# Performance work log

Hardware: AMD Instinct MI355X
Metric: run time of the kernel (lower is better)

## Reference

```python
import jax, jax.numpy as jnp
import numpy as np

L, V, D = 8, 512, 256            # num_loci, per-locus vocab, embedding_dim
B, K = 8192, 16                  # batch, candidates per sample
HID = 2 * D                      # pooling MLP hidden width


def setup_inputs() -> dict:
    key = jax.random.key(0)
    k_tok, k_tab, k_w1, k_w2 = jax.random.split(key, 4)
    haplotypes = jax.random.randint(k_tok, (B, K, L), 0, V, dtype=jnp.int64)
    # nn.Embedding default init: N(0, 1); padding_idx row zeroed.
    tables = jax.random.normal(k_tab, (L, V, D), dtype=jnp.float32)
    tables = tables.at[:, 0, :].set(0.0)
    # Xavier-uniform for the two Linear layers (stored as [in, out]).
    lim1 = float(np.sqrt(6.0 / (L * D + HID)))
    W1 = jax.random.uniform(k_w1, (L * D, HID), jnp.float32, -lim1, lim1)
    b1 = jnp.zeros((HID,), jnp.float32)
    lim2 = float(np.sqrt(6.0 / (HID + D)))
    W2 = jax.random.uniform(k_w2, (HID, D), jnp.float32, -lim2, lim2)
    b2 = jnp.zeros((D,), jnp.float32)
    return {"haplotypes": haplotypes, "tables": tables,
            "W1": W1, "b1": b1, "W2": W2, "b2": b2}


def reference(haplotypes, tables, W1, b1, W2, b2):
    b, k, num_loci = haplotypes.shape
    vocab = tables.shape[1]
    tok = jnp.clip(haplotypes.reshape(-1, num_loci), 0, vocab - 1)  # [N, L]
    # Per-locus gather, vectorized over loci: [N, L, D]
    emb = tables[jnp.arange(num_loci), tok]
    # padding_idx row is all-zeros; masking keeps forward identical and
    # matches torch's zero-gradient behavior for the padding row.
    emb = emb * (tok != 0)[..., None].astype(emb.dtype)
    x = emb.reshape(emb.shape[0], num_loci * tables.shape[2])  # concat -> [N, L*D]
    h = jax.nn.gelu(x @ W1 + b1, approximate=False)            # torch GELU = erf
    out = h @ W2 + b2                                          # [N, D]
    return out.reshape(b, k, tables.shape[2])
```

## Files before the change

kernel.cpp:

```cpp
#include <hip/hip_runtime.h>
#include <math.h>

typedef __attribute__((ext_vector_type(8))) short  short8;
typedef __attribute__((ext_vector_type(4))) float  floatx4;
typedef __attribute__((ext_vector_type(2))) float  float2v;
typedef __attribute__((ext_vector_type(4))) unsigned int uintx4;

#define NLOCI 8
#define VOCAB 512
#define DDIM  256
#define HID   512
#define NSAMP (8192 * 16)

__device__ __forceinline__ float bitsf(unsigned int u) {
    union { unsigned int u; float f; } c; c.u = u; return c.f;
}
__device__ __forceinline__ unsigned short f2bf(float f) {
    union { float f; unsigned int u; } c; c.f = f;
    unsigned int u = c.u;
    return (unsigned short)((u + 0x7FFFu + ((u >> 16) & 1u)) >> 16);
}
__device__ __forceinline__ unsigned short f2bf_fast(float f) {
    union { float f; unsigned int u; } c; c.f = f;
    return (unsigned short)((c.u + 0x8000u) >> 16);
}
__device__ __forceinline__ float gelu_fast(float x) {
    float t = x * x;
    float y = x * __builtin_fmaf(0.035677408f, t, 0.79788456f);
    float e = __builtin_amdgcn_exp2f(y * 2.8853901f);
    float r = __builtin_amdgcn_rcpf(e + 1.0f);
    return x - x * r;
}
__device__ __forceinline__ void async_copy16(const void* g, void* l) {
    __builtin_amdgcn_global_load_lds(
        (const __attribute__((address_space(1))) unsigned int*)g,
        (__attribute__((address_space(3))) unsigned int*)l, 16, 0, 0);
}

__device__ __forceinline__ short8 sum_gelu(const uintx4* g) {
    short8 afrag;
#pragma unroll
    for (int j = 0; j < 4; ++j) {
        float2v u0 = (float2v){bitsf(g[0][j] << 16), bitsf(g[0][j] & 0xFFFF0000u)};
        float2v u1 = (float2v){bitsf(g[1][j] << 16), bitsf(g[1][j] & 0xFFFF0000u)};
        float2v u2 = (float2v){bitsf(g[2][j] << 16), bitsf(g[2][j] & 0xFFFF0000u)};
        float2v u3 = (float2v){bitsf(g[3][j] << 16), bitsf(g[3][j] & 0xFFFF0000u)};
        float2v u4 = (float2v){bitsf(g[4][j] << 16), bitsf(g[4][j] & 0xFFFF0000u)};
        float2v u5 = (float2v){bitsf(g[5][j] << 16), bitsf(g[5][j] & 0xFFFF0000u)};
        float2v u6 = (float2v){bitsf(g[6][j] << 16), bitsf(g[6][j] & 0xFFFF0000u)};
        float2v u7 = (float2v){bitsf(g[7][j] << 16), bitsf(g[7][j] & 0xFFFF0000u)};
        float2v sj = ((u0 + u1) + (u2 + u3)) + ((u4 + u5) + (u6 + u7));
        afrag[2 * j]     = (short)f2bf_fast(gelu_fast(sj[0]));
        afrag[2 * j + 1] = (short)f2bf_fast(gelu_fast(sj[1]));
    }
    return afrag;
}

__global__ __launch_bounds__(256) void k_prep(
    const float* __restrict__ tables,
    const float* __restrict__ W1,
    const float* __restrict__ b1,
    const float* __restrict__ W2,
    unsigned short* __restrict__ Tp,
    unsigned short* __restrict__ W2t)
{
    __shared__ unsigned short a_lds[64 * 256];
    __shared__ unsigned short bt_lds[64 * 256];

    const int t = threadIdx.x;

    if (blockIdx.x >= 512) {
        const int bid = blockIdx.x - 512;
        const int r0 = (bid & 7) * 64;
        const int c0 = (bid >> 3) * 64;
        float* tile = (float*)a_lds;
#pragma unroll
        for (int i = 0; i < 16; ++i) {
            int flat = i * 256 + t;
            int rr = flat >> 6, cc = flat & 63;
            tile[rr * 65 + cc] = W2[(r0 + rr) * DDIM + c0 + cc];
        }
        __syncthreads();
#pragma unroll
        for (int i = 0; i < 8; ++i) {
            int flat = i * 256 + t;
            int cc = flat >> 5, rp = (flat & 31) * 2;
            ushort2 v;
            v.x = f2bf(tile[rp * 65 + cc]);
            v.y = f2bf(tile[(rp + 1) * 65 + cc]);
            *(ushort2*)(W2t + (c0 + cc) * HID + r0 + rp) = v;
        }
        return;
    }

    const int l  = blockIdx.x >> 6;
    const int v0 = ((blockIdx.x >> 3) & 7) * 64;
    const int n0 = (blockIdx.x & 7) * 64;

    {
        const float* asrc = tables + (l * 512 + v0) * 256;
#pragma unroll
        for (int i = 0; i < 16; ++i) {
            int flat = i * 1024 + t * 4;
            int row = flat >> 8, k = flat & 255;
            float4 v = *(const float4*)(asrc + flat);
            ushort4 pk4;
            pk4.x = f2bf(v.x); pk4.y = f2bf(v.y); pk4.z = f2bf(v.z); pk4.w = f2bf(v.w);
            int chunkX = (k >> 3) ^ (row & 31);
            *(ushort4*)(a_lds + row * 256 + chunkX * 8 + (k & 7)) = pk4;
        }
    }
    {
        const int n = t & 63;
        const int kq = (t >> 6) * 64;
        const float* bsrc = W1 + (l * 256) * 512 + n0 + n;
#pragma unroll
        for (int i = 0; i < 8; ++i) {
            int k0 = kq + i * 8;
            short8 pk8;
#pragma unroll
            for (int j = 0; j < 8; ++j)
                pk8[j] = (short)f2bf(bsrc[(k0 + j) * 512]);
            int chunkX = (k0 >> 3) ^ (n & 31);
            *(short8*)(bt_lds + n * 256 + chunkX * 8) = pk8;
        }
    }
    __syncthreads();

    const int wave = t >> 6, lane = t & 63;
    const int p = lane & 15, q = lane >> 4;
    const int arow = wave * 16 + p;

    floatx4 acc[4];
#pragma unroll
    for (int nt = 0; nt < 4; ++nt) acc[nt] = (floatx4){0.f, 0.f, 0.f, 0.f};

#pragma unroll
    for (int kc = 0; kc < 8; ++kc) {
        int cq = kc * 4 + q;
        short8 afrag = *(const short8*)(a_lds + arow * 256 + (cq ^ (arow & 31)) * 8);
#pragma unroll
        for (int nt = 0; nt < 4; ++nt) {
            int brow = nt * 16 + p;
            short8 bfrag = *(const short8*)(bt_lds + brow * 256 + (cq ^ (brow & 31)) * 8);
            acc[nt] = __builtin_amdgcn_mfma_f32_16x16x32_bf16(afrag, bfrag, acc[nt], 0, 0, 0);
        }
    }

#pragma unroll
    for (int nt = 0; nt < 4; ++nt) {
        int col = n0 + nt * 16 + p;
        float badd = (l == 0) ? b1[col] : 0.0f;
#pragma unroll
        for (int r = 0; r < 4; ++r) {
            int row = v0 + wave * 16 + q * 4 + r;
            Tp[(l * 512 + row) * 512 + col] = f2bf(acc[nt][r] + badd);
        }
    }
}

__global__ __launch_bounds__(256, 3) void k_main(
    const int* __restrict__ hap,
    const unsigned short* __restrict__ Tp,
    const unsigned short* __restrict__ W2t,
    const float* __restrict__ b2,
    float* __restrict__ out)
{
    __shared__ unsigned short w2_lds[256 * 64];

    const int t = threadIdx.x;
    const int wave = t >> 6, lane = t & 63;
    const int p = lane & 15, q = lane >> 4;
    const int m_base = blockIdx.x * 64 + wave * 16;

    unsigned int goff[8];
    {
        const uintx4* hp = (const uintx4*)(hap + (m_base + p) * 8);
        uintx4 h0 = hp[0], h1 = hp[1];
#pragma unroll
        for (int l = 0; l < 4; ++l) {
            goff[l]     = (unsigned)(l)     * 524288u + (h0[l] & 511u) * 1024u + (unsigned)(q * 32);
            goff[l + 4] = (unsigned)(l + 4) * 524288u + (h1[l] & 511u) * 1024u + (unsigned)(q * 32);
        }
    }
    const char* Tpc = (const char*)Tp;

    const int drow = lane >> 3;
    const int j_sw = (lane & 7) ^ (drow & 7);
    const unsigned short* wsrc = W2t + (wave * 64 + drow) * 512 + j_sw * 8;
    const int p7 = p & 7;

    floatx4 acc[16];
#pragma unroll
    for (int nt = 0; nt < 16; ++nt) acc[nt] = (floatx4){0.f, 0.f, 0.f, 0.f};

    uintx4 ga0[8], ga1[8];
#pragma unroll
    for (int l = 0; l < 8; ++l)
        ga0[l] = *(const uintx4*)(Tpc + goff[l]);
#pragma unroll
    for (int l = 0; l < 8; ++l)
        ga1[l] = *(const uintx4*)(Tpc + goff[l] + 16);
    __builtin_amdgcn_sched_barrier(0);

#pragma unroll
    for (int kb = 0; kb < 8; ++kb) {
        asm volatile("s_waitcnt lgkmcnt(0)" ::: "memory");
        __builtin_amdgcn_s_barrier();
        __builtin_amdgcn_sched_barrier(0);
#pragma unroll
        for (int i = 0; i < 8; ++i)
            async_copy16(wsrc + kb * 64 + i * 8 * 512,
                         w2_lds + (wave * 64 + i * 8) * 64);
        __builtin_amdgcn_sched_barrier(0);

        asm volatile("s_waitcnt vmcnt(16)" ::: "memory");
        short8 afrag0 = sum_gelu(ga0);
        __builtin_amdgcn_sched_barrier(0);

        if (kb < 7) {
#pragma unroll
            for (int l = 0; l < 8; ++l)
                ga0[l] = *(const uintx4*)(Tpc + goff[l] + (kb + 1) * 128);
            __builtin_amdgcn_sched_barrier(0);
        }

        if (kb < 7) { asm volatile("s_waitcnt vmcnt(8)" ::: "memory"); }
        else        { asm volatile("s_waitcnt vmcnt(0)" ::: "memory"); }
        __builtin_amdgcn_s_barrier();
        __builtin_amdgcn_sched_barrier(0);

        {
            const unsigned short* b0 = w2_lds + p * 64 + (((q << 1) ^ p7) * 8);
            __builtin_amdgcn_s_setprio(1);
#pragma unroll
            for (int nt = 0; nt < 16; ++nt) {
                short8 bfrag = *(const short8*)(b0 + nt * 1024);
                acc[nt] = __builtin_amdgcn_mfma_f32_16x16x32_bf16(afrag0, bfrag, acc[nt], 0, 0, 0);
            }
            __builtin_amdgcn_s_setprio(0);
        }

        short8 afrag1 = sum_gelu(ga1);
        __builtin_amdgcn_sched_barrier(0);
        if (kb < 7) {
#pragma unroll
            for (int l = 0; l < 8; ++l)
                ga1[l] = *(const uintx4*)(Tpc + goff[l] + (kb + 1) * 128 + 16);
            __builtin_amdgcn_sched_barrier(0);
        }
        {
            const unsigned short* b1p = w2_lds + p * 64 + ((((q << 1) | 1) ^ p7) * 8);
            __builtin_amdgcn_s_setprio(1);
#pragma unroll
            for (int nt = 0; nt < 16; ++nt) {
                short8 bfrag = *(const short8*)(b1p + nt * 1024);
                acc[nt] = __builtin_amdgcn_mfma_f32_16x16x32_bf16(afrag1, bfrag, acc[nt], 0, 0, 0);
            }
            __builtin_amdgcn_s_setprio(0);
        }
    }

#pragma unroll
    for (int nt = 0; nt < 16; ++nt) {
        int n = nt * 16 + p;
        float b2v = b2[n];
#pragma unroll
        for (int r = 0; r < 4; ++r) {
            int m = m_base + q * 4 + r;
            __builtin_nontemporal_store(acc[nt][r] + b2v, out + m * 256 + n);
        }
    }
}

extern "C" void kernel_launch(void* const* d_in, const int* in_sizes, int n_in,
                              void* d_out, int out_size, void* d_ws, size_t ws_size,
                              hipStream_t stream) {
    const int*   hap    = (const int*)d_in[0];
    const float* tables = (const float*)d_in[1];
    const float* W1     = (const float*)d_in[2];
    const float* b1     = (const float*)d_in[3];
    const float* W2     = (const float*)d_in[4];
    const float* b2     = (const float*)d_in[5];
    float*       outp   = (float*)d_out;

    unsigned short* Tp  = (unsigned short*)d_ws;
    unsigned short* W2t = (unsigned short*)d_ws + NLOCI * VOCAB * HID;

    k_prep<<<dim3(544), dim3(256), 0, stream>>>(tables, W1, b1, W2, Tp, W2t);
    k_main<<<dim3(NSAMP / 64), dim3(256), 0, stream>>>(hap, Tp, W2t, b2, outp);
}
```

Before: 287.9 us.

## Single-buffer gathered rows and raise main kernel occupancy to 4 blocks

Replaces the two 8-register-vector gather buffers with a single buffer reused between the two k-halves, and raises launch bounds from 3 to 4 blocks per CU. The W2 LDS copy is permuted so the K-chunk each fragment reads matches the new load order. The aim is to free enough VGPRs for higher occupancy, at the cost of less in-flight prefetch per wave, because each gather now has to finish before the next one is issued.

```diff
diff --git a/kernel.cpp b/kernel.cpp
--- a/kernel.cpp
+++ b/kernel.cpp
@@ -159,7 +159,7 @@
     }
 }
 
-__global__ __launch_bounds__(256, 3) void k_main(
+__global__ __launch_bounds__(256, 4) void k_main(
     const int* __restrict__ hap,
     const unsigned short* __restrict__ Tp,
     const unsigned short* __restrict__ W2t,
@@ -186,21 +186,19 @@
     const char* Tpc = (const char*)Tp;
 
     const int drow = lane >> 3;
-    const int j_sw = (lane & 7) ^ (drow & 7);
-    const unsigned short* wsrc = W2t + (wave * 64 + drow) * 512 + j_sw * 8;
+    const int jx = (lane & 7) ^ (drow & 7);
+    const int c_src = (((jx << 1) | (jx >> 2)) & 7);
+    const unsigned short* wsrc = W2t + (wave * 64 + drow) * 512 + c_src * 8;
     const int p7 = p & 7;
 
     floatx4 acc[16];
 #pragma unroll
     for (int nt = 0; nt < 16; ++nt) acc[nt] = (floatx4){0.f, 0.f, 0.f, 0.f};
 
-    uintx4 ga0[8], ga1[8];
+    uintx4 gbuf[8];
 #pragma unroll
     for (int l = 0; l < 8; ++l)
-        ga0[l] = *(const uintx4*)(Tpc + goff[l]);
-#pragma unroll
-    for (int l = 0; l < 8; ++l)
-        ga1[l] = *(const uintx4*)(Tpc + goff[l] + 16);
+        gbuf[l] = *(const uintx4*)(Tpc + goff[l]);
     __builtin_amdgcn_sched_barrier(0);
 
 #pragma unroll
@@ -214,24 +212,21 @@
                          w2_lds + (wave * 64 + i * 8) * 64);
         __builtin_amdgcn_sched_barrier(0);
 
-        asm volatile("s_waitcnt vmcnt(16)" ::: "memory");
-        short8 afrag0 = sum_gelu(ga0);
-        __builtin_amdgcn_sched_barrier(0);
-
-        if (kb < 7) {
-#pragma unroll
-            for (int l = 0; l < 8; ++l)
-                ga0[l] = *(const uintx4*)(Tpc + goff[l] + (kb + 1) * 128);
-            __builtin_amdgcn_sched_barrier(0);
-        }
-
-        if (kb < 7) { asm volatile("s_waitcnt vmcnt(8)" ::: "memory"); }
-        else        { asm volatile("s_waitcnt vmcnt(0)" ::: "memory"); }
+        asm volatile("s_waitcnt vmcnt(8)" ::: "memory");
+        short8 afrag0 = sum_gelu(gbuf);
+        __builtin_amdgcn_sched_barrier(0);
+
+#pragma unroll
+        for (int l = 0; l < 8; ++l)
+            gbuf[l] = *(const uintx4*)(Tpc + goff[l] + kb * 128 + 16);
+        __builtin_amdgcn_sched_barrier(0);
+
+        asm volatile("s_waitcnt vmcnt(8)" ::: "memory");
         __builtin_amdgcn_s_barrier();
         __builtin_amdgcn_sched_barrier(0);
 
         {
-            const unsigned short* b0 = w2_lds + p * 64 + (((q << 1) ^ p7) * 8);
+            const unsigned short* b0 = w2_lds + p * 64 + ((q ^ p7) * 8);
             __builtin_amdgcn_s_setprio(1);
 #pragma unroll
             for (int nt = 0; nt < 16; ++nt) {
@@ -241,16 +236,19 @@
             __builtin_amdgcn_s_setprio(0);
         }
 
-        short8 afrag1 = sum_gelu(ga1);
-        __builtin_amdgcn_sched_barrier(0);
+        asm volatile("s_waitcnt vmcnt(0)" ::: "memory");
+        short8 afrag1 = sum_gelu(gbuf);
+        __builtin_amdgcn_sched_barrier(0);
+
         if (kb < 7) {
 #pragma unroll
             for (int l = 0; l < 8; ++l)
-                ga1[l] = *(const uintx4*)(Tpc + goff[l] + (kb + 1) * 128 + 16);
+                gbuf[l] = *(const uintx4*)(Tpc + goff[l] + (kb + 1) * 128);
             __builtin_amdgcn_sched_barrier(0);
         }
+
         {
-            const unsigned short* b1p = w2_lds + p * 64 + ((((q << 1) | 1) ^ p7) * 8);
+            const unsigned short* b1p = w2_lds + p * 64 + (((4 + q) ^ p7) * 8);
             __builtin_amdgcn_s_setprio(1);
 #pragma unroll
             for (int nt = 0; nt < 16; ++nt) {
```

New measurement: 307.3 us. +6.7%, slower.
